# Optimization experiments

Hardware: AMD Instinct MI355X
Metric: run time of the kernel (lower is better)

The kernel has to match this reference:

```python
import jax, jax.numpy as jnp
import numpy as np

N_UP, N_DOWN, M, D, K, F, L, B = 16, 16, 4, 128, 64, 32, 3, 1024
N = N_UP + N_DOWN
H_W = 45  # round(sqrt(F*K)), hidden dim of the 2-layer w MLP
LOG2 = float(np.log(2.0))


def ssp(x):
    # shifted softplus activation used by deepqmc
    return jax.nn.softplus(x) - LOG2


def _pair_blocks(n_up, n_down):
    # replicate idx_perm(N,2) grouped by i, then idx_pair_spin partition
    n = n_up + n_down
    i = np.repeat(np.arange(n), n - 1)
    j = np.concatenate([np.concatenate([np.arange(k), np.arange(k + 1, n)]) for k in range(n)])
    blocks = []
    for mi, mj, ri, rj in [(True, True, n_up, max(n_up - 1, 0)),
                           (True, False, n_up, n_down),
                           (False, True, n_down, n_up),
                           (False, False, n_down, max(n_down - 1, 0))]:
        mask = ((i < n_up) == mi) & ((j < n_up) == mj)
        blocks.append((i[mask].reshape(ri, rj), j[mask].reshape(ri, rj)))
    return blocks

_BLOCKS = _pair_blocks(N_UP, N_DOWN)
_CHANS = [0, 1, 1, 0]  # same, anti, anti, same (w/g channel index; 2 = nuclear)


def setup_inputs() -> dict:
    key = jax.random.key(0)
    ks = jax.random.split(key, 12)
    s = 0.1
    return {
        'edges_elec': jax.random.normal(ks[0], (B, N, N, F), jnp.float32),
        'edges_nuc': jax.random.normal(ks[1], (B, N, M, F), jnp.float32),
        'X': jax.random.normal(ks[2], (1, D), jnp.float32) * s,
        'Y': jax.random.normal(ks[3], (M, K), jnp.float32) * s,
        'wW1': jax.random.normal(ks[4], (L, 3, H_W, F), jnp.float32) * s,
        'wb1': jax.random.normal(ks[5], (L, 3, H_W), jnp.float32) * s,
        'wW2': jax.random.normal(ks[6], (L, 3, K, H_W), jnp.float32) * s,
        'wb2': jax.random.normal(ks[7], (L, 3, K), jnp.float32) * s,
        'hW': jax.random.normal(ks[8], (L, K, D), jnp.float32) * s,
        'hb': jax.random.normal(ks[9], (L, K), jnp.float32) * s,
        'gW': jax.random.normal(ks[10], (L, 3, D, K), jnp.float32) * s,
        'gb': jax.random.normal(ks[11], (L, 3, D), jnp.float32) * s,
    }


def reference(edges_elec, edges_nuc, X, Y, wW1, wb1, wW2, wb2, hW, hb, gW, gb):
    def w_mlp(l, c, e):
        # 2-layer log-dim MLP: F -> H_W -> K with SSP in between
        return ssp(e @ wW1[l, c].T + wb1[l, c]) @ wW2[l, c].T + wb2[l, c]

    b = edges_nuc.shape[0]
    x = jnp.broadcast_to(X, (b, N, D))  # initial electron embeddings (n_up==n_down)
    for l in range(L):
        h = x @ hW[l].T + hb[l]  # shared h subnet: [b,N,K]
        zs = []
        for (ii, jj), c in zip(_BLOCKS, _CHANS):
            e = edges_elec[:, ii, jj, :]               # [b, ri, rj, F] gather
            msg = w_mlp(l, c, e) * h[:, jj, :]          # [b, ri, rj, K]
            zs.append(msg.sum(axis=-2))                 # segment-sum over j
        z_same = jnp.concatenate([zs[0], zs[3]], axis=-2)  # up then down
        z_anti = jnp.concatenate([zs[1], zs[2]], axis=-2)
        z_nuc = jnp.einsum('bnmk,mk->bnk', w_mlp(l, 2, edges_nuc), Y)
        update = (z_same @ gW[l, 0].T + gb[l, 0]
                  + z_anti @ gW[l, 1].T + gb[l, 1]
                  + z_nuc @ gW[l, 2].T + gb[l, 2])
        x = x + update  # resnet
    return x
```

## Files before the change

### kernel.cpp

```cpp
#include <hip/hip_runtime.h>
#include <math.h>

#define N_   32
#define NUP_ 16
#define M_   4
#define D_   128
#define K_   64
#define F_   32
#define H_   45
#define L_   3
#define LOG2_ 0.69314718055994530942f

typedef __attribute__((ext_vector_type(8))) short short8;
typedef __attribute__((ext_vector_type(4))) float float4v;

__device__ __forceinline__ float ssp(float v) {
    return __logf(1.0f + __expf(v)) - LOG2_;
}

__device__ __forceinline__ unsigned short f2bf(float x) {
    unsigned int u = __float_as_uint(x);
    return (unsigned short)((u + 0x7FFFu + ((u >> 16) & 1u)) >> 16);
}

__device__ __forceinline__ unsigned int pkbf(float x, float y) {
    return __builtin_amdgcn_perm(__float_as_uint(y) + 0x8000u,
                                 __float_as_uint(x) + 0x8000u, 0x07060302u);
}

__global__ __launch_bounds__(256) void prep_kernel(
    const float* __restrict__ wW1, const float* __restrict__ wW2,
    const float* __restrict__ wb2, const float* __restrict__ gW,
    const float* __restrict__ hW,  const float* __restrict__ gb,
    short* __restrict__ w1B, short* __restrict__ w2B,
    short* __restrict__ gB,  short* __restrict__ hB, float* __restrict__ gbs)
{
    int blk = blockIdx.x;
    int t = threadIdx.x;
    if (blk < 27) {
        int lc = blk / 3, nt = blk % 3;
        short* dst = w1B + (size_t)blk * 512;
        for (int idx = t; idx < 512; idx += 256) {
            int lane = idx >> 3, jj = idx & 7;
            int k = ((lane >> 4) << 3) + jj;
            int n = nt * 16 + (lane & 15);
            float v = (n < H_) ? wW1[((size_t)lc * H_ + n) * F_ + k] : 0.0f;
            dst[idx] = (short)f2bf(v);
        }
    } else if (blk < 99) {
        int b3 = blk - 27;
        int lc = b3 >> 3, rem = b3 & 7, ks = rem >> 2, nt = rem & 3;
        short* dst = w2B + (size_t)b3 * 512;
        for (int idx = t; idx < 512; idx += 256) {
            int lane = idx >> 3, jj = idx & 7;
            int p = ks * 32 + ((lane >> 4) << 3) + jj;
            int n = nt * 16 + (lane & 15);
            float v;
            if (p == 3) v = wb2[(size_t)lc * K_ + n];
            else if ((p & 3) < 3) {
                int u = (p & 3) * 16 + (p >> 2);
                v = (u < H_) ? wW2[((size_t)lc * K_ + n) * H_ + u] : 0.0f;
            } else v = 0.0f;
            dst[idx] = (short)f2bf(v);
        }
    } else if (blk < 243) {
        int g = blk - 99;
        int l = g / 48, rem = g % 48;
        short* dst = gB + (size_t)g * 512;
        for (int idx = t; idx < 512; idx += 256) {
            int lane = idx >> 3, jj = idx & 7;
            int k = (rem >> 3) * 32 + ((lane >> 4) << 3) + jj;
            int c = k >> 6, kk = k & 63;
            int n = ((rem & 7) * 16) + (lane & 15);
            dst[idx] = (short)f2bf(gW[(((size_t)l * 3 + c) * D_ + n) * K_ + kk]);
        }
    } else if (blk < 275) {
        int hh = blk - 243;
        int li = hh >> 4, rem = hh & 15;
        short* dst = hB + (size_t)hh * 512;
        for (int idx = t; idx < 512; idx += 256) {
            int lane = idx >> 3, jj = idx & 7;
            int d = (rem >> 2) * 32 + ((lane >> 4) << 3) + jj;
            int n = ((rem & 3) * 16) + (lane & 15);
            dst[idx] = (short)f2bf(hW[(((size_t)(li + 1)) * K_ + n) * D_ + d]);
        }
    } else {
        for (int idx = t; idx < 384; idx += 256) {
            int l = idx >> 7, d = idx & 127;
            gbs[idx] = gb[((size_t)l * 3 + 0) * D_ + d]
                     + gb[((size_t)l * 3 + 1) * D_ + d]
                     + gb[((size_t)l * 3 + 2) * D_ + d];
        }
    }
}

__global__ __launch_bounds__(64) void h0_kernel(
    const float* __restrict__ X, const float* __restrict__ hW,
    const float* __restrict__ hb, float* __restrict__ h0)
{
    int k = threadIdx.x;
    float a = hb[k];
    const float* w = hW + (size_t)k * D_;
    #pragma unroll 8
    for (int dd = 0; dd < D_; ++dd) a += w[dd] * X[dd];
    h0[k] = a;
}

#define HDS 72
__global__ __launch_bounds__(512, 5) void edge_kernel(
    const float* __restrict__ ee, const float* __restrict__ en,
    const float* __restrict__ Y,
    const short* __restrict__ w1B, const float* __restrict__ wb1,
    const short* __restrict__ w2B,
    const float* __restrict__ h, const float* __restrict__ h0,
    unsigned short* __restrict__ zb, int l, int hmode)
{
    __shared__ float wrowT[36 * 64];
    __shared__ short hd_s[8][16 * HDS];
    __shared__ float part_s[8][256];

    const int tid  = threadIdx.x;
    const int wv   = tid >> 6;
    const int lane = tid & 63;
    const int quad = lane >> 4;
    const int l16  = lane & 15;
    const int b    = blockIdx.x >> 2;
    const int i    = ((blockIdx.x & 3) << 3) + wv;
    const int bi   = (b << 5) + i;

    {
        int row = tid >> 4;
        int c0 = (tid & 15) * 4;
        int m = c0 >> 4, lb = c0 & 15;
        const float* src = hmode ? (h + ((size_t)(b * N_ + row)) * K_ + c0) : (h0 + c0);
        float4 v = *(const float4*)src;
        wrowT[row * 64 + (lb + 0) * 4 + m] = v.x;
        wrowT[row * 64 + (lb + 1) * 4 + m] = v.y;
        wrowT[row * 64 + (lb + 2) * 4 + m] = v.z;
        wrowT[row * 64 + (lb + 3) * 4 + m] = v.w;
        if (tid < 64) {
            int r2 = 32 + (tid >> 4);
            float4 y = *(const float4*)(Y + ((size_t)(tid >> 4)) * K_ + c0);
            wrowT[r2 * 64 + (lb + 0) * 4 + m] = y.x;
            wrowT[r2 * 64 + (lb + 1) * 4 + m] = y.y;
            wrowT[r2 * 64 + (lb + 2) * 4 + m] = y.z;
            wrowT[r2 * 64 + (lb + 3) * 4 + m] = y.w;
        }
    }
    __syncthreads();

    const int cA = (i < NUP_) ? 0 : 1;
    const int cs0 = cA, cs1 = 1 - cA, cs2 = 2;
    short* hd = hd_s[wv];
    float* part = part_s[wv];
    const unsigned int cpad = (l16 == 0) ? 0x3F808000u : 0u;

    const float* ep = ee + (((size_t)bi * N_) + l16) * F_ + quad * 8;
    float4 e0a = *(const float4*)(ep);
    float4 e0b = *(const float4*)(ep + 4);
    float4 e1a = *(const float4*)(ep + 16 * F_);
    float4 e1b = *(const float4*)(ep + 16 * F_ + 4);
    float4 e2a = {0.f,0.f,0.f,0.f}, e2b = {0.f,0.f,0.f,0.f};
    if (l16 < M_) {
        const float* np = en + (((size_t)bi * M_) + l16) * F_ + quad * 8;
        e2a = *(const float4*)(np);
        e2b = *(const float4*)(np + 4);
    }
    float b1r[9];
    {
        const int cls[3] = {l * 3 + cs0, l * 3 + cs1, l * 3 + cs2};
        #pragma unroll
        for (int t = 0; t < 3; ++t)
            #pragma unroll
            for (int nt = 0; nt < 3; ++nt) {
                int col = nt * 16 + l16;
                b1r[t * 3 + nt] = (col < H_) ? wb1[(size_t)cls[t] * H_ + col] : 0.0f;
            }
    }
    union { short8 s; unsigned int u[4]; } A[3];
    A[0].u[0] = pkbf(e0a.x, e0a.y); A[0].u[1] = pkbf(e0a.z, e0a.w);
    A[0].u[2] = pkbf(e0b.x, e0b.y); A[0].u[3] = pkbf(e0b.z, e0b.w);
    A[1].u[0] = pkbf(e1a.x, e1a.y); A[1].u[1] = pkbf(e1a.z, e1a.w);
    A[1].u[2] = pkbf(e1b.x, e1b.y); A[1].u[3] = pkbf(e1b.z, e1b.w);
    A[2].u[0] = pkbf(e2a.x, e2a.y); A[2].u[1] = pkbf(e2a.z, e2a.w);
    A[2].u[2] = pkbf(e2b.x, e2b.y); A[2].u[3] = pkbf(e2b.z, e2b.w);

    #pragma unroll
    for (int t = 0; t < 3; ++t) {
        const int c  = (t == 0) ? cs0 : ((t == 1) ? cs1 : cs2);
        const int lc = l * 3 + c;

        float4v acc1[3];
        #pragma unroll
        for (int nt = 0; nt < 3; ++nt) {
            float b1c = b1r[t * 3 + nt];
            acc1[nt] = (float4v){b1c, b1c, b1c, b1c};
            short8 bf = *(const short8*)(w1B + (((size_t)lc * 3 + nt) << 9) + (lane << 3));
            acc1[nt] = __builtin_amdgcn_mfma_f32_16x16x32_bf16(A[t].s, bf, acc1[nt], 0, 0, 0);
        }

        #pragma unroll
        for (int r = 0; r < 4; ++r) {
            float s0 = ssp(acc1[0][r]);
            float s1 = ssp(acc1[1][r]);
            float s2 = ssp(acc1[2][r]);
            unsigned int lo = pkbf(s0, s1);
            unsigned int hi = __builtin_amdgcn_perm(cpad, __float_as_uint(s2) + 0x8000u, 0x07060302u);
            uint2 pr; pr.x = lo; pr.y = hi;
            *(uint2*)(hd + (quad * 4 + r) * HDS + 4 * l16) = pr;
        }

        float4v acc2[4];
        #pragma unroll
        for (int nt = 0; nt < 4; ++nt) acc2[nt] = (float4v){0.f, 0.f, 0.f, 0.f};
        #pragma unroll
        for (int ks = 0; ks < 2; ++ks) {
            short8 a2 = *(const short8*)(hd + l16 * HDS + ks * 32 + quad * 8);
            #pragma unroll
            for (int nt = 0; nt < 4; ++nt) {
                short8 bf = *(const short8*)(w2B + ((((size_t)lc * 2 + ks) * 4 + nt) << 9) + (lane << 3));
                acc2[nt] = __builtin_amdgcn_mfma_f32_16x16x32_bf16(a2, bf, acc2[nt], 0, 0, 0);
            }
        }

        float p0 = 0.f, p1 = 0.f, p2 = 0.f, p3 = 0.f;
        #pragma unroll
        for (int r = 0; r < 4; ++r) {
            int jrow = t * 16 + quad * 4 + r;
            int jcl = (jrow < 36) ? jrow : 35;
            float4 wv4 = *(const float4*)(wrowT + jcl * 64 + l16 * 4);
            bool live = (t == 2) ? (jrow < 36) : (jrow != i);
            if (!live) { wv4.x = 0.f; wv4.y = 0.f; wv4.z = 0.f; wv4.w = 0.f; }
            p0 += acc2[0][r] * wv4.x;
            p1 += acc2[1][r] * wv4.y;
            p2 += acc2[2][r] * wv4.z;
            p3 += acc2[3][r] * wv4.w;
        }
        float4 pv; pv.x = p0; pv.y = p1; pv.z = p2; pv.w = p3;
        *(float4*)(&part[(quad * 16 + l16) * 4]) = pv;
        __builtin_amdgcn_s_waitcnt(0);
        float zsum = part[l16 * 4 + quad] + part[64 + l16 * 4 + quad]
                   + part[128 + l16 * 4 + quad] + part[192 + l16 * 4 + quad];
        zb[(size_t)bi * 192 + c * 64 + lane] =
            (unsigned short)((__float_as_uint(zsum) + 0x8000u) >> 16);
    }
}

#define XPS 132
#define HXS 136
__global__ __launch_bounds__(192, 4) void fuse_kernel(
    const unsigned short* __restrict__ zb, const short* __restrict__ gB,
    const float* __restrict__ gbs, const float* __restrict__ X,
    const short* __restrict__ hB, const float* __restrict__ hb,
    float* __restrict__ xout, float* __restrict__ hout,
    int l, int first, int compute_h)
{
    __shared__ float xpart[3][16 * XPS];
    __shared__ short hx[16 * HXS];

    const int tid  = threadIdx.x;
    const int wv   = tid >> 6;
    const int lane = tid & 63;
    const int quad = lane >> 4;
    const int l16  = lane & 15;
    const int bi0  = blockIdx.x * 16;

    float4v ax[8];
    #pragma unroll
    for (int nt = 0; nt < 8; ++nt) ax[nt] = (float4v){0.f, 0.f, 0.f, 0.f};
    const short* zrow = (const short*)zb + ((size_t)(bi0 + l16)) * 192;
    const short* gl = gB + (size_t)l * 48 * 512;
    #pragma unroll
    for (int ks2 = 0; ks2 < 2; ++ks2) {
        int ks = wv * 2 + ks2;
        short8 az = *(const short8*)(zrow + ks * 32 + quad * 8);
        #pragma unroll
        for (int nt = 0; nt < 8; ++nt) {
            short8 bf = *(const short8*)(gl + (((size_t)ks * 8 + nt) << 9) + (lane << 3));
            ax[nt] = __builtin_amdgcn_mfma_f32_16x16x32_bf16(az, bf, ax[nt], 0, 0, 0);
        }
    }
    float* xp = xpart[wv];
    #pragma unroll
    for (int r = 0; r < 4; ++r) {
        int row = quad * 4 + r;
        float4 lo; lo.x = ax[0][r]; lo.y = ax[1][r]; lo.z = ax[2][r]; lo.w = ax[3][r];
        float4 hi; hi.x = ax[4][r]; hi.y = ax[5][r]; hi.z = ax[6][r]; hi.w = ax[7][r];
        *(float4*)(&xp[row * XPS + l16 * 8])     = lo;
        *(float4*)(&xp[row * XPS + l16 * 8 + 4]) = hi;
    }
    __syncthreads();

    if (tid < 128) {
        int row = tid >> 3, nt = tid & 7;
        int dbase = nt * 16;
        size_t gi = ((size_t)(bi0 + row)) * D_ + dbase;
        float acc[16];
        #pragma unroll
        for (int j = 0; j < 16; ++j) {
            int o = row * XPS + j * 8 + nt;
            acc[j] = xpart[0][o] + xpart[1][o] + xpart[2][o];
        }
        float res[16];
        #pragma unroll
        for (int q = 0; q < 4; ++q) {
            float4 rv = first ? *(const float4*)(X + dbase + q * 4)
                              : *(const float4*)(xout + gi + q * 4);
            float4 gv = *(const float4*)(gbs + (size_t)l * D_ + dbase + q * 4);
            res[q*4+0] = rv.x + gv.x; res[q*4+1] = rv.y + gv.y;
            res[q*4+2] = rv.z + gv.z; res[q*4+3] = rv.w + gv.w;
        }
        float xo[16];
        #pragma unroll
        for (int j = 0; j < 16; ++j) xo[j] = acc[j] + res[j];
        #pragma unroll
        for (int q = 0; q < 4; ++q) {
            float4 sv; sv.x = xo[q*4+0]; sv.y = xo[q*4+1]; sv.z = xo[q*4+2]; sv.w = xo[q*4+3];
            *(float4*)(xout + gi + q * 4) = sv;
        }
        if (compute_h) {
            union { short8 s; unsigned int u[4]; } P0, P1;
            P0.u[0] = pkbf(xo[0], xo[1]);  P0.u[1] = pkbf(xo[2], xo[3]);
            P0.u[2] = pkbf(xo[4], xo[5]);  P0.u[3] = pkbf(xo[6], xo[7]);
            P1.u[0] = pkbf(xo[8], xo[9]);  P1.u[1] = pkbf(xo[10], xo[11]);
            P1.u[2] = pkbf(xo[12], xo[13]); P1.u[3] = pkbf(xo[14], xo[15]);
            *(short8*)(hx + row * HXS + dbase)     = P0.s;
            *(short8*)(hx + row * HXS + dbase + 8) = P1.s;
        }
    }
    if (!compute_h) return;
    __syncthreads();

    float4v ah[4];
    #pragma unroll
    for (int nt = 0; nt < 4; ++nt) ah[nt] = (float4v){0.f, 0.f, 0.f, 0.f};
    const short* hl = hB + (size_t)l * 16 * 512;
    #pragma unroll
    for (int ks = 0; ks < 4; ++ks) {
        short8 a = *(const short8*)(hx + l16 * HXS + ks * 32 + quad * 8);
        #pragma unroll
        for (int nt = 0; nt < 4; ++nt) {
            short8 bf = *(const short8*)(hl + (((size_t)ks * 4 + nt) << 9) + (lane << 3));
            ah[nt] = __builtin_amdgcn_mfma_f32_16x16x32_bf16(a, bf, ah[nt], 0, 0, 0);
        }
    }
    int nlo = (wv == 0) ? 0 : ((wv == 1) ? 2 : 3);
    int nhi = (wv == 0) ? 2 : (nlo + 1);
    for (int nt = nlo; nt < nhi; ++nt) {
        float hbv = hb[((size_t)(l + 1)) * K_ + nt * 16 + l16];
        #pragma unroll
        for (int r = 0; r < 4; ++r)
            hout[((size_t)(bi0 + quad * 4 + r)) * K_ + nt * 16 + l16] = ah[nt][r] + hbv;
    }
}

extern "C" void kernel_launch(void* const* d_in, const int* in_sizes, int n_in,
                              void* d_out, int out_size, void* d_ws, size_t ws_size,
                              hipStream_t stream)
{
    const float* ee  = (const float*)d_in[0];
    const float* en  = (const float*)d_in[1];
    const float* X   = (const float*)d_in[2];
    const float* Y   = (const float*)d_in[3];
    const float* wW1 = (const float*)d_in[4];
    const float* wb1 = (const float*)d_in[5];
    const float* wW2 = (const float*)d_in[6];
    const float* wb2 = (const float*)d_in[7];
    const float* hW  = (const float*)d_in[8];
    const float* hb  = (const float*)d_in[9];
    const float* gW  = (const float*)d_in[10];
    const float* gb  = (const float*)d_in[11];
    float* xout = (float*)d_out;

    char* ws = (char*)d_ws;
    float*          h   = (float*)(ws);
    unsigned short* zb  = (unsigned short*)(ws + 8388608);
    float*          h0  = (float*)(ws + 8388608 + 12582912);
    short*          w1B = (short*)(ws + 20971520 + 256);
    short*          w2B = w1B + (size_t)27 * 512;
    short*          gB  = w2B + (size_t)72 * 512;
    short*          hB  = gB  + (size_t)144 * 512;
    float*          gbs = (float*)(hB + (size_t)32 * 512);

    prep_kernel<<<276, 256, 0, stream>>>(wW1, wW2, wb2, gW, hW, gb,
                                         w1B, w2B, gB, hB, gbs);
    h0_kernel<<<1, 64, 0, stream>>>(X, hW, hb, h0);

    edge_kernel<<<4096, 512, 0, stream>>>(ee, en, Y, w1B, wb1, w2B, h, h0, zb, 0, 0);
    fuse_kernel<<<2048, 192, 0, stream>>>(zb, gB, gbs, X, hB, hb, xout, h, 0, 1, 1);
    edge_kernel<<<4096, 512, 0, stream>>>(ee, en, Y, w1B, wb1, w2B, h, h0, zb, 1, 1);
    fuse_kernel<<<2048, 192, 0, stream>>>(zb, gB, gbs, X, hB, hb, xout, h, 1, 0, 1);
    edge_kernel<<<4096, 512, 0, stream>>>(ee, en, Y, w1B, wb1, w2B, h, h0, zb, 2, 1);
    fuse_kernel<<<2048, 192, 0, stream>>>(zb, gB, gbs, X, hB, hb, xout, h, 2, 0, 0);
}
```

Before: 452.7 us.

## Restructure edge kernel per batch and split fuse kernel across column halves

The edge kernel now gives each block a whole batch element, with each wave looping over 4 electrons. The h tile is staged once per batch instead of per 8 electrons. The nuclear MLP is batched across 4 electrons in one MFMA tile. The per-wave LDS partial reduction is replaced by cross-lane shuffles, and the diagonal j==i is masked in the hidden activations. The fuse kernel drops the cross-wave LDS K-split reduction: each wave computes the full K for 4 output column tiles over 32 rows. The risks are fewer, longer-lived blocks and a serial ii loop that limits latency hiding.

```diff
diff --git a/kernel.cpp b/kernel.cpp
--- a/kernel.cpp
+++ b/kernel.cpp
@@ -107,7 +107,7 @@
 }
 
 #define HDS 72
-__global__ __launch_bounds__(512, 5) void edge_kernel(
+__global__ __launch_bounds__(512, 6) void edge_kernel(
     const float* __restrict__ ee, const float* __restrict__ en,
     const float* __restrict__ Y,
     const short* __restrict__ w1B, const float* __restrict__ wb1,
@@ -115,90 +115,155 @@
     const float* __restrict__ h, const float* __restrict__ h0,
     unsigned short* __restrict__ zb, int l, int hmode)
 {
-    __shared__ float wrowT[36 * 64];
+    __shared__ float wrowT[32 * 64];
+    __shared__ float yT[16 * 20];
     __shared__ short hd_s[8][16 * HDS];
-    __shared__ float part_s[8][256];
 
     const int tid  = threadIdx.x;
     const int wv   = tid >> 6;
     const int lane = tid & 63;
     const int quad = lane >> 4;
     const int l16  = lane & 15;
-    const int b    = blockIdx.x >> 2;
-    const int i    = ((blockIdx.x & 3) << 3) + wv;
-    const int bi   = (b << 5) + i;
+    const int b    = blockIdx.x;
 
     {
         int row = tid >> 4;
         int c0 = (tid & 15) * 4;
-        int m = c0 >> 4, lb = c0 & 15;
         const float* src = hmode ? (h + ((size_t)(b * N_ + row)) * K_ + c0) : (h0 + c0);
         float4 v = *(const float4*)src;
-        wrowT[row * 64 + (lb + 0) * 4 + m] = v.x;
-        wrowT[row * 64 + (lb + 1) * 4 + m] = v.y;
-        wrowT[row * 64 + (lb + 2) * 4 + m] = v.z;
-        wrowT[row * 64 + (lb + 3) * 4 + m] = v.w;
+        wrowT[row * 64 + ((c0 + 0) & 15) * 4 + ((c0 + 0) >> 4)] = v.x;
+        wrowT[row * 64 + ((c0 + 1) & 15) * 4 + ((c0 + 1) >> 4)] = v.y;
+        wrowT[row * 64 + ((c0 + 2) & 15) * 4 + ((c0 + 2) >> 4)] = v.z;
+        wrowT[row * 64 + ((c0 + 3) & 15) * 4 + ((c0 + 3) >> 4)] = v.w;
         if (tid < 64) {
-            int r2 = 32 + (tid >> 4);
-            float4 y = *(const float4*)(Y + ((size_t)(tid >> 4)) * K_ + c0);
-            wrowT[r2 * 64 + (lb + 0) * 4 + m] = y.x;
-            wrowT[r2 * 64 + (lb + 1) * 4 + m] = y.y;
-            wrowT[r2 * 64 + (lb + 2) * 4 + m] = y.z;
-            wrowT[r2 * 64 + (lb + 3) * 4 + m] = y.w;
+            int yl = tid & 15, g = tid >> 4;
+            float4 yv;
+            yv.x = Y[0 * K_ + g * 16 + yl];
+            yv.y = Y[1 * K_ + g * 16 + yl];
+            yv.z = Y[2 * K_ + g * 16 + yl];
+            yv.w = Y[3 * K_ + g * 16 + yl];
+            *(float4*)(yT + yl * 20 + g * 4) = yv;
         }
     }
     __syncthreads();
 
-    const int cA = (i < NUP_) ? 0 : 1;
-    const int cs0 = cA, cs1 = 1 - cA, cs2 = 2;
+    const int i0  = wv * 4;
+    const int cA  = (wv < 4) ? 0 : 1;
+    const int lc0 = l * 3 + cA;
+    const int lc1 = l * 3 + 1 - cA;
+    const int lc2 = l * 3 + 2;
     short* hd = hd_s[wv];
-    float* part = part_s[wv];
     const unsigned int cpad = (l16 == 0) ? 0x3F808000u : 0u;
 
-    const float* ep = ee + (((size_t)bi * N_) + l16) * F_ + quad * 8;
-    float4 e0a = *(const float4*)(ep);
-    float4 e0b = *(const float4*)(ep + 4);
-    float4 e1a = *(const float4*)(ep + 16 * F_);
-    float4 e1b = *(const float4*)(ep + 16 * F_ + 4);
-    float4 e2a = {0.f,0.f,0.f,0.f}, e2b = {0.f,0.f,0.f,0.f};
-    if (l16 < M_) {
-        const float* np = en + (((size_t)bi * M_) + l16) * F_ + quad * 8;
-        e2a = *(const float4*)(np);
-        e2b = *(const float4*)(np + 4);
-    }
     float b1r[9];
     {
-        const int cls[3] = {l * 3 + cs0, l * 3 + cs1, l * 3 + cs2};
+        const int lcs[3] = {lc0, lc1, lc2};
         #pragma unroll
         for (int t = 0; t < 3; ++t)
             #pragma unroll
             for (int nt = 0; nt < 3; ++nt) {
                 int col = nt * 16 + l16;
-                b1r[t * 3 + nt] = (col < H_) ? wb1[(size_t)cls[t] * H_ + col] : 0.0f;
-            }
-    }
-    union { short8 s; unsigned int u[4]; } A[3];
-    A[0].u[0] = pkbf(e0a.x, e0a.y); A[0].u[1] = pkbf(e0a.z, e0a.w);
-    A[0].u[2] = pkbf(e0b.x, e0b.y); A[0].u[3] = pkbf(e0b.z, e0b.w);
-    A[1].u[0] = pkbf(e1a.x, e1a.y); A[1].u[1] = pkbf(e1a.z, e1a.w);
-    A[1].u[2] = pkbf(e1b.x, e1b.y); A[1].u[3] = pkbf(e1b.z, e1b.w);
-    A[2].u[0] = pkbf(e2a.x, e2a.y); A[2].u[1] = pkbf(e2a.z, e2a.w);
-    A[2].u[2] = pkbf(e2b.x, e2b.y); A[2].u[3] = pkbf(e2b.z, e2b.w);
-
-    #pragma unroll
-    for (int t = 0; t < 3; ++t) {
-        const int c  = (t == 0) ? cs0 : ((t == 1) ? cs1 : cs2);
-        const int lc = l * 3 + c;
+                b1r[t * 3 + nt] = (col < H_) ? wb1[(size_t)lcs[t] * H_ + col] : 0.0f;
+            }
+    }
+
+    for (int ii = 0; ii < 4; ++ii) {
+        const int i = i0 + ii;
+        const size_t bi = (size_t)b * N_ + i;
+
+        const float* ep = ee + (bi * N_ + l16) * F_ + quad * 8;
+        float4 e0a = *(const float4*)(ep);
+        float4 e0b = *(const float4*)(ep + 4);
+        float4 e1a = *(const float4*)(ep + 16 * F_);
+        float4 e1b = *(const float4*)(ep + 16 * F_ + 4);
+        union { short8 s; unsigned int u[4]; } A[2];
+        A[0].u[0] = pkbf(e0a.x, e0a.y); A[0].u[1] = pkbf(e0a.z, e0a.w);
+        A[0].u[2] = pkbf(e0b.x, e0b.y); A[0].u[3] = pkbf(e0b.z, e0b.w);
+        A[1].u[0] = pkbf(e1a.x, e1a.y); A[1].u[1] = pkbf(e1a.z, e1a.w);
+        A[1].u[2] = pkbf(e1b.x, e1b.y); A[1].u[3] = pkbf(e1b.z, e1b.w);
+
+        const int lct[2] = {lc0, lc1};
+        const int dtile = i >> 4;
+
+        #pragma unroll
+        for (int t = 0; t < 2; ++t) {
+            const int lc = lct[t];
+
+            float4v acc1[3];
+            #pragma unroll
+            for (int nt = 0; nt < 3; ++nt) {
+                float b1c = b1r[t * 3 + nt];
+                acc1[nt] = (float4v){b1c, b1c, b1c, b1c};
+                short8 bf = *(const short8*)(w1B + (((size_t)lc * 3 + nt) << 9) + (lane << 3));
+                acc1[nt] = __builtin_amdgcn_mfma_f32_16x16x32_bf16(A[t].s, bf, acc1[nt], 0, 0, 0);
+            }
+
+            const int drow = (t == dtile) ? (i & 15) : 99;
+            #pragma unroll
+            for (int r = 0; r < 4; ++r) {
+                float s0 = ssp(acc1[0][r]);
+                float s1 = ssp(acc1[1][r]);
+                float s2 = ssp(acc1[2][r]);
+                unsigned int lo = pkbf(s0, s1);
+                unsigned int hi = __builtin_amdgcn_perm(cpad, __float_as_uint(s2) + 0x8000u, 0x07060302u);
+                if (quad * 4 + r == drow) { lo = 0u; hi = 0u; }
+                uint2 pr; pr.x = lo; pr.y = hi;
+                *(uint2*)(hd + (quad * 4 + r) * HDS + 4 * l16) = pr;
+            }
+
+            float4v acc2[4];
+            #pragma unroll
+            for (int nt = 0; nt < 4; ++nt) acc2[nt] = (float4v){0.f, 0.f, 0.f, 0.f};
+            #pragma unroll
+            for (int ks = 0; ks < 2; ++ks) {
+                short8 a2 = *(const short8*)(hd + l16 * HDS + ks * 32 + quad * 8);
+                #pragma unroll
+                for (int nt = 0; nt < 4; ++nt) {
+                    short8 bf = *(const short8*)(w2B + ((((size_t)lc * 2 + ks) * 4 + nt) << 9) + (lane << 3));
+                    acc2[nt] = __builtin_amdgcn_mfma_f32_16x16x32_bf16(a2, bf, acc2[nt], 0, 0, 0);
+                }
+            }
+
+            float p0 = 0.f, p1 = 0.f, p2 = 0.f, p3 = 0.f;
+            #pragma unroll
+            for (int r = 0; r < 4; ++r) {
+                int jrow = t * 16 + quad * 4 + r;
+                float4 wv4 = *(const float4*)(wrowT + jrow * 64 + l16 * 4);
+                p0 += acc2[0][r] * wv4.x;
+                p1 += acc2[1][r] * wv4.y;
+                p2 += acc2[2][r] * wv4.z;
+                p3 += acc2[3][r] * wv4.w;
+            }
+            p0 += __shfl_xor(p0, 16); p0 += __shfl_xor(p0, 32);
+            p1 += __shfl_xor(p1, 16); p1 += __shfl_xor(p1, 32);
+            p2 += __shfl_xor(p2, 16); p2 += __shfl_xor(p2, 32);
+            p3 += __shfl_xor(p3, 16); p3 += __shfl_xor(p3, 32);
+            float v = p0;
+            v = (quad == 1) ? p1 : v;
+            v = (quad == 2) ? p2 : v;
+            v = (quad == 3) ? p3 : v;
+            const int cch = (t == 0) ? cA : 1 - cA;
+            zb[bi * 192 + cch * 64 + lane] =
+                (unsigned short)((__float_as_uint(v) + 0x8000u) >> 16);
+        }
+    }
+
+    {
+        const float* np = en + (((size_t)b * N_ + i0 + (l16 >> 2)) * M_ + (l16 & 3)) * F_ + quad * 8;
+        float4 na = *(const float4*)(np);
+        float4 nb = *(const float4*)(np + 4);
+        union { short8 s; unsigned int u[4]; } An;
+        An.u[0] = pkbf(na.x, na.y); An.u[1] = pkbf(na.z, na.w);
+        An.u[2] = pkbf(nb.x, nb.y); An.u[3] = pkbf(nb.z, nb.w);
 
         float4v acc1[3];
         #pragma unroll
         for (int nt = 0; nt < 3; ++nt) {
-            float b1c = b1r[t * 3 + nt];
+            float b1c = b1r[6 + nt];
             acc1[nt] = (float4v){b1c, b1c, b1c, b1c};
-            short8 bf = *(const short8*)(w1B + (((size_t)lc * 3 + nt) << 9) + (lane << 3));
-            acc1[nt] = __builtin_amdgcn_mfma_f32_16x16x32_bf16(A[t].s, bf, acc1[nt], 0, 0, 0);
-        }
-
+            short8 bf = *(const short8*)(w1B + (((size_t)lc2 * 3 + nt) << 9) + (lane << 3));
+            acc1[nt] = __builtin_amdgcn_mfma_f32_16x16x32_bf16(An.s, bf, acc1[nt], 0, 0, 0);
+        }
         #pragma unroll
         for (int r = 0; r < 4; ++r) {
             float s0 = ssp(acc1[0][r]);
@@ -209,7 +274,6 @@
             uint2 pr; pr.x = lo; pr.y = hi;
             *(uint2*)(hd + (quad * 4 + r) * HDS + 4 * l16) = pr;
         }
-
         float4v acc2[4];
         #pragma unroll
         for (int nt = 0; nt < 4; ++nt) acc2[nt] = (float4v){0.f, 0.f, 0.f, 0.f};
@@ -218,139 +282,93 @@
             short8 a2 = *(const short8*)(hd + l16 * HDS + ks * 32 + quad * 8);
             #pragma unroll
             for (int nt = 0; nt < 4; ++nt) {
-                short8 bf = *(const short8*)(w2B + ((((size_t)lc * 2 + ks) * 4 + nt) << 9) + (lane << 3));
+                short8 bf = *(const short8*)(w2B + ((((size_t)lc2 * 2 + ks) * 4 + nt) << 9) + (lane << 3));
                 acc2[nt] = __builtin_amdgcn_mfma_f32_16x16x32_bf16(a2, bf, acc2[nt], 0, 0, 0);
             }
         }
-
-        float p0 = 0.f, p1 = 0.f, p2 = 0.f, p3 = 0.f;
-        #pragma unroll
-        for (int r = 0; r < 4; ++r) {
-            int jrow = t * 16 + quad * 4 + r;
-            int jcl = (jrow < 36) ? jrow : 35;
-            float4 wv4 = *(const float4*)(wrowT + jcl * 64 + l16 * 4);
-            bool live = (t == 2) ? (jrow < 36) : (jrow != i);
-            if (!live) { wv4.x = 0.f; wv4.y = 0.f; wv4.z = 0.f; wv4.w = 0.f; }
-            p0 += acc2[0][r] * wv4.x;
-            p1 += acc2[1][r] * wv4.y;
-            p2 += acc2[2][r] * wv4.z;
-            p3 += acc2[3][r] * wv4.w;
-        }
-        float4 pv; pv.x = p0; pv.y = p1; pv.z = p2; pv.w = p3;
-        *(float4*)(&part[(quad * 16 + l16) * 4]) = pv;
-        __builtin_amdgcn_s_waitcnt(0);
-        float zsum = part[l16 * 4 + quad] + part[64 + l16 * 4 + quad]
-                   + part[128 + l16 * 4 + quad] + part[192 + l16 * 4 + quad];
-        zb[(size_t)bi * 192 + c * 64 + lane] =
-            (unsigned short)((__float_as_uint(zsum) + 0x8000u) >> 16);
-    }
-}
-
-#define XPS 132
-#define HXS 136
-__global__ __launch_bounds__(192, 4) void fuse_kernel(
+        size_t zbase = ((size_t)b * N_ + i0 + quad) * 192 + 128 + l16;
+        #pragma unroll
+        for (int nt = 0; nt < 4; ++nt) {
+            float4 yv = *(const float4*)(yT + l16 * 20 + nt * 4);
+            float p = acc2[nt][0] * yv.x + acc2[nt][1] * yv.y
+                    + acc2[nt][2] * yv.z + acc2[nt][3] * yv.w;
+            zb[zbase + nt * 16] = (unsigned short)((__float_as_uint(p) + 0x8000u) >> 16);
+        }
+    }
+}
+
+#define HXS2 136
+__global__ __launch_bounds__(256) void fuse_kernel(
     const unsigned short* __restrict__ zb, const short* __restrict__ gB,
     const float* __restrict__ gbs, const float* __restrict__ X,
     const short* __restrict__ hB, const float* __restrict__ hb,
     float* __restrict__ xout, float* __restrict__ hout,
     int l, int first, int compute_h)
 {
-    __shared__ float xpart[3][16 * XPS];
-    __shared__ short hx[16 * HXS];
+    __shared__ short hx[32 * HXS2];
 
     const int tid  = threadIdx.x;
-    const int wv   = tid >> 6;
+    const int wvv  = tid >> 6;
+    const int r2   = wvv & 1;
+    const int nh   = wvv >> 1;
     const int lane = tid & 63;
     const int quad = lane >> 4;
     const int l16  = lane & 15;
-    const int bi0  = blockIdx.x * 16;
-
-    float4v ax[8];
+    const int row0 = blockIdx.x * 32 + r2 * 16;
+
+    float4v acc[4];
     #pragma unroll
-    for (int nt = 0; nt < 8; ++nt) ax[nt] = (float4v){0.f, 0.f, 0.f, 0.f};
-    const short* zrow = (const short*)zb + ((size_t)(bi0 + l16)) * 192;
+    for (int n = 0; n < 4; ++n) acc[n] = (float4v){0.f, 0.f, 0.f, 0.f};
+    const short* zrow = (const short*)zb + (size_t)(row0 + l16) * 192;
     const short* gl = gB + (size_t)l * 48 * 512;
     #pragma unroll
-    for (int ks2 = 0; ks2 < 2; ++ks2) {
-        int ks = wv * 2 + ks2;
+    for (int ks = 0; ks < 6; ++ks) {
         short8 az = *(const short8*)(zrow + ks * 32 + quad * 8);
         #pragma unroll
-        for (int nt = 0; nt < 8; ++nt) {
-            short8 bf = *(const short8*)(gl + (((size_t)ks * 8 + nt) << 9) + (lane << 3));
-            ax[nt] = __builtin_amdgcn_mfma_f32_16x16x32_bf16(az, bf, ax[nt], 0, 0, 0);
-        }
-    }
-    float* xp = xpart[wv];
+        for (int n = 0; n < 4; ++n) {
+            short8 bf = *(const short8*)(gl + ((size_t)(ks * 8 + nh * 4 + n) << 9) + (lane << 3));
+            acc[n] = __builtin_amdgcn_mfma_f32_16x16x32_bf16(az, bf, acc[n], 0, 0, 0);
+        }
+    }
+
     #pragma unroll
-    for (int r = 0; r < 4; ++r) {
-        int row = quad * 4 + r;
-        float4 lo; lo.x = ax[0][r]; lo.y = ax[1][r]; lo.z = ax[2][r]; lo.w = ax[3][r];
-        float4 hi; hi.x = ax[4][r]; hi.y = ax[5][r]; hi.z = ax[6][r]; hi.w = ax[7][r];
-        *(float4*)(&xp[row * XPS + l16 * 8])     = lo;
-        *(float4*)(&xp[row * XPS + l16 * 8 + 4]) = hi;
-    }
-    __syncthreads();
-
-    if (tid < 128) {
-        int row = tid >> 3, nt = tid & 7;
-        int dbase = nt * 16;
-        size_t gi = ((size_t)(bi0 + row)) * D_ + dbase;
-        float acc[16];
-        #pragma unroll
-        for (int j = 0; j < 16; ++j) {
-            int o = row * XPS + j * 8 + nt;
-            acc[j] = xpart[0][o] + xpart[1][o] + xpart[2][o];
-        }
-        float res[16];
-        #pragma unroll
-        for (int q = 0; q < 4; ++q) {
-            float4 rv = first ? *(const float4*)(X + dbase + q * 4)
-                              : *(const float4*)(xout + gi + q * 4);
-            float4 gv = *(const float4*)(gbs + (size_t)l * D_ + dbase + q * 4);
-            res[q*4+0] = rv.x + gv.x; res[q*4+1] = rv.y + gv.y;
-            res[q*4+2] = rv.z + gv.z; res[q*4+3] = rv.w + gv.w;
-        }
-        float xo[16];
-        #pragma unroll
-        for (int j = 0; j < 16; ++j) xo[j] = acc[j] + res[j];
-        #pragma unroll
-        for (int q = 0; q < 4; ++q) {
-            float4 sv; sv.x = xo[q*4+0]; sv.y = xo[q*4+1]; sv.z = xo[q*4+2]; sv.w = xo[q*4+3];
-            *(float4*)(xout + gi + q * 4) = sv;
-        }
-        if (compute_h) {
-            union { short8 s; unsigned int u[4]; } P0, P1;
-            P0.u[0] = pkbf(xo[0], xo[1]);  P0.u[1] = pkbf(xo[2], xo[3]);
-            P0.u[2] = pkbf(xo[4], xo[5]);  P0.u[3] = pkbf(xo[6], xo[7]);
-            P1.u[0] = pkbf(xo[8], xo[9]);  P1.u[1] = pkbf(xo[10], xo[11]);
-            P1.u[2] = pkbf(xo[12], xo[13]); P1.u[3] = pkbf(xo[14], xo[15]);
-            *(short8*)(hx + row * HXS + dbase)     = P0.s;
-            *(short8*)(hx + row * HXS + dbase + 8) = P1.s;
+    for (int n = 0; n < 4; ++n) {
+        int col = (nh * 4 + n) * 16 + l16;
+        float gv = gbs[(size_t)l * D_ + col];
+        float xbc = first ? X[col] : 0.0f;
+        #pragma unroll
+        for (int r = 0; r < 4; ++r) {
+            size_t gi = (size_t)(row0 + quad * 4 + r) * D_ + col;
+            float xo = (first ? xbc : xout[gi]) + gv + acc[n][r];
+            xout[gi] = xo;
+            if (compute_h)
+                hx[(r2 * 16 + quad * 4 + r) * HXS2 + col] =
+                    (short)((__float_as_uint(xo) + 0x8000u) >> 16);
         }
     }
     if (!compute_h) return;
     __syncthreads();
 
-    float4v ah[4];
-    #pragma unroll
-    for (int nt = 0; nt < 4; ++nt) ah[nt] = (float4v){0.f, 0.f, 0.f, 0.f};
+    float4v ah[2];
+    ah[0] = (float4v){0.f, 0.f, 0.f, 0.f};
+    ah[1] = (float4v){0.f, 0.f, 0.f, 0.f};
     const short* hl = hB + (size_t)l * 16 * 512;
     #pragma unroll
     for (int ks = 0; ks < 4; ++ks) {
-        short8 a = *(const short8*)(hx + l16 * HXS + ks * 32 + quad * 8);
-        #pragma unroll
-        for (int nt = 0; nt < 4; ++nt) {
-            short8 bf = *(const short8*)(hl + (((size_t)ks * 4 + nt) << 9) + (lane << 3));
-            ah[nt] = __builtin_amdgcn_mfma_f32_16x16x32_bf16(a, bf, ah[nt], 0, 0, 0);
-        }
-    }
-    int nlo = (wv == 0) ? 0 : ((wv == 1) ? 2 : 3);
-    int nhi = (wv == 0) ? 2 : (nlo + 1);
-    for (int nt = nlo; nt < nhi; ++nt) {
-        float hbv = hb[((size_t)(l + 1)) * K_ + nt * 16 + l16];
+        short8 a = *(const short8*)(hx + (r2 * 16 + l16) * HXS2 + ks * 32 + quad * 8);
+        #pragma unroll
+        for (int n = 0; n < 2; ++n) {
+            short8 bf = *(const short8*)(hl + ((size_t)(ks * 4 + nh * 2 + n) << 9) + (lane << 3));
+            ah[n] = __builtin_amdgcn_mfma_f32_16x16x32_bf16(a, bf, ah[n], 0, 0, 0);
+        }
+    }
+    #pragma unroll
+    for (int n = 0; n < 2; ++n) {
+        int kc = (nh * 2 + n) * 16 + l16;
+        float hbv = hb[((size_t)(l + 1)) * K_ + kc];
         #pragma unroll
         for (int r = 0; r < 4; ++r)
-            hout[((size_t)(bi0 + quad * 4 + r)) * K_ + nt * 16 + l16] = ah[nt][r] + hbv;
+            hout[(size_t)(row0 + quad * 4 + r) * K_ + kc] = ah[n][r] + hbv;
     }
 }
 
@@ -386,10 +404,10 @@
                                          w1B, w2B, gB, hB, gbs);
     h0_kernel<<<1, 64, 0, stream>>>(X, hW, hb, h0);
 
-    edge_kernel<<<4096, 512, 0, stream>>>(ee, en, Y, w1B, wb1, w2B, h, h0, zb, 0, 0);
-    fuse_kernel<<<2048, 192, 0, stream>>>(zb, gB, gbs, X, hB, hb, xout, h, 0, 1, 1);
-    edge_kernel<<<4096, 512, 0, stream>>>(ee, en, Y, w1B, wb1, w2B, h, h0, zb, 1, 1);
-    fuse_kernel<<<2048, 192, 0, stream>>>(zb, gB, gbs, X, hB, hb, xout, h, 1, 0, 1);
-    edge_kernel<<<4096, 512, 0, stream>>>(ee, en, Y, w1B, wb1, w2B, h, h0, zb, 2, 1);
-    fuse_kernel<<<2048, 192, 0, stream>>>(zb, gB, gbs, X, hB, hb, xout, h, 2, 0, 0);
-}
+    edge_kernel<<<1024, 512, 0, stream>>>(ee, en, Y, w1B, wb1, w2B, h, h0, zb, 0, 0);
+    fuse_kernel<<<1024, 256, 0, stream>>>(zb, gB, gbs, X, hB, hb, xout, h, 0, 1, 1);
+    edge_kernel<<<1024, 512, 0, stream>>>(ee, en, Y, w1B, wb1, w2B, h, h0, zb, 1, 1);
+    fuse_kernel<<<1024, 256, 0, stream>>>(zb, gB, gbs, X, hB, hb, xout, h, 1, 0, 1);
+    edge_kernel<<<1024, 512, 0, stream>>>(ee, en, Y, w1B, wb1, w2B, h, h0, zb, 2, 1);
+    fuse_kernel<<<1024, 256, 0, stream>>>(zb, gB, gbs, X, hB, hb, xout, h, 2, 0, 0);
+}
```

Result: slower. 1.018 ms (+125.0%).
